# Kernel optimization log

Measured on AMD Instinct MI355X. Metric: run time of the kernel, lower is better.

## Reference

```python
import jax, jax.numpy as jnp
import numpy as np

B, N, CIN, C = 2, 400000, 192, 128
Y, X, Z = 512, 512, 40
EPS1 = 1e-5   # default BatchNorm1d eps for feature_proj
EPS2 = 1e-3   # norm_fn eps=0.001 for shared_conv BN


def setup_inputs() -> dict:
    key = jax.random.key(0)
    ks = jax.random.split(key, 12)
    voxel_features = jax.random.normal(ks[0], (N, CIN), jnp.float32)
    bi = jax.random.randint(ks[1], (N,), 0, B)
    zi = jax.random.randint(ks[2], (N,), 0, Z)
    yi = jax.random.randint(ks[3], (N,), 0, Y)
    xi = jax.random.randint(ks[4], (N,), 0, X)
    voxel_coords = jnp.stack([bi, zi, yi, xi], axis=1).astype(jnp.int32)  # (N,4)=[b,z,y,x]
    # feature_proj: Linear(CIN->C) + BN1d (inference stats) + ReLU
    W_proj = jax.random.normal(ks[5], (CIN, C), jnp.float32) * np.float32(1.0 / np.sqrt(CIN))
    b_proj = jnp.zeros((C,), jnp.float32)
    bn1_gamma = jnp.ones((C,), jnp.float32)
    bn1_beta = jnp.zeros((C,), jnp.float32)
    bn1_mean = jax.random.normal(ks[6], (C,), jnp.float32) * np.float32(0.1)
    bn1_var = jax.random.uniform(ks[7], (C,), jnp.float32, 0.5, 1.5)
    # shared_conv: SubMConv2d(C,C,3,pad=1,bias) + BN(eps=1e-3) + ReLU
    conv_w = jax.random.normal(ks[8], (3, 3, C, C), jnp.float32) * np.float32(1.0 / np.sqrt(9 * C))
    conv_b = jnp.zeros((C,), jnp.float32)
    bn2_gamma = jnp.ones((C,), jnp.float32)
    bn2_beta = jnp.zeros((C,), jnp.float32)
    bn2_mean = jax.random.normal(ks[9], (C,), jnp.float32) * np.float32(0.1)
    bn2_var = jax.random.uniform(ks[10], (C,), jnp.float32, 0.5, 1.5)
    return dict(voxel_features=voxel_features, voxel_coords=voxel_coords,
                W_proj=W_proj, b_proj=b_proj,
                bn1_gamma=bn1_gamma, bn1_beta=bn1_beta, bn1_mean=bn1_mean, bn1_var=bn1_var,
                conv_w=conv_w, conv_b=conv_b,
                bn2_gamma=bn2_gamma, bn2_beta=bn2_beta, bn2_mean=bn2_mean, bn2_var=bn2_var)


def reference(voxel_features, voxel_coords, W_proj, b_proj,
              bn1_gamma, bn1_beta, bn1_mean, bn1_var,
              conv_w, conv_b, bn2_gamma, bn2_beta, bn2_mean, bn2_var):
    # 1) feature_proj (Linear + BN1d inference + ReLU)
    f = voxel_features @ W_proj + b_proj                      # (N, C)
    f = (f - bn1_mean) * jax.lax.rsqrt(bn1_var + EPS1) * bn1_gamma + bn1_beta
    f = jax.nn.relu(f)
    # 2) bev_aggregate: unique([b,y,x]) + index_add == scatter-sum to dense BEV grid
    bi, yi, xi = voxel_coords[:, 0], voxel_coords[:, 2], voxel_coords[:, 3]
    dense = jnp.zeros((B, Y, X, C), f.dtype).at[bi, yi, xi].add(f)
    active = jnp.zeros((B, Y, X), bool).at[bi, yi, xi].set(True)
    # 3) SubMConv2d(3x3, pad=1) + BN + ReLU; subm == dense conv masked to active sites
    out = jax.lax.conv_general_dilated(dense, conv_w, (1, 1), 'SAME',
                                       dimension_numbers=('NHWC', 'HWIO', 'NHWC')) + conv_b
    out = (out - bn2_mean) * jax.lax.rsqrt(bn2_var + EPS2) * bn2_gamma + bn2_beta
    out = jax.nn.relu(out)
    # sparse tensor only holds active sites; zero elsewhere
    return jnp.where(active[..., None], out, jnp.float32(0.0))  # (B, Y, X, C)
```

## Files before the change

### kernel.cpp

```cpp
#include <hip/hip_runtime.h>

#define Bq 2
#define Yq 512
#define Xq 512
#define NVOX 400000

typedef __bf16 bf16x8 __attribute__((ext_vector_type(8)));
typedef float f32x4 __attribute__((ext_vector_type(4)));
typedef float f32x16 __attribute__((ext_vector_type(16)));
typedef short s16x8 __attribute__((ext_vector_type(8)));
typedef short s16x2 __attribute__((ext_vector_type(2)));

__device__ __forceinline__ short f2bf_s(float f){
    return __builtin_bit_cast(short, static_cast<__bf16>(f));
}

__device__ __forceinline__ void atomic_pk_add_bf16(short* addr, unsigned data){
#if __has_builtin(__builtin_amdgcn_global_atomic_fadd_v2bf16)
    s16x2 v; v[0] = (short)(data & 0xffff); v[1] = (short)(data >> 16);
    __builtin_amdgcn_global_atomic_fadd_v2bf16(
        (__attribute__((address_space(1))) s16x2*)addr, v);
#else
    asm volatile("global_atomic_pk_add_bf16 %0, %1, off"
                 :: "v"(addr), "v"(data) : "memory");
#endif
}

__global__ void kprep(const float* __restrict__ conv_w, const float* __restrict__ W_proj,
                      short* __restrict__ wTs, short* __restrict__ wpT){
    int tid = blockIdx.x*256 + threadIdx.x;
    if (tid < 9*128*128){
        int tap = tid >> 14; int r = tid & 16383; int co = r >> 7; int ci = r & 127;
        int g = ci >> 3, e = ci & 7;
        wTs[tap*16384 + co*128 + (((g & 8) | ((g & 7) ^ (co & 7))) << 3) + e] =
            f2bf_s(conv_w[tap*16384 + ci*128 + co]);
    }
    int e = tid - 9*128*128;
    if (e >= 0 && e < 128*192){
        int co = e / 192; int ci = e - co*192;
        wpT[e] = f2bf_s(W_proj[ci*128 + co]);
    }
}

__global__ void kcount(const int* __restrict__ vc, unsigned* __restrict__ cnt,
                       unsigned char* __restrict__ act){
    int i = blockIdx.x*256 + threadIdx.x;
    if (i >= NVOX) return;
    const int4 c = *reinterpret_cast<const int4*>(vc + i*4);
    int cell = (c.x*Yq + c.z)*Xq + c.w;
    act[cell] = 1;
    atomicAdd(&cnt[cell], 1u);
}

__global__ void __launch_bounds__(256, 4)
kproj(const float* __restrict__ vf, const int* __restrict__ vc,
      const unsigned* __restrict__ cnt,
      const short* __restrict__ wpT, const float* __restrict__ bp,
      const float* __restrict__ g1, const float* __restrict__ be1,
      const float* __restrict__ mu1, const float* __restrict__ va1,
      short* __restrict__ dbf){
    __shared__ char smem[64*200*2];
    __shared__ int cellsPk[64];
    short*    A  = (short*)smem;
    unsigned* st = (unsigned*)smem;
    const int t = threadIdx.x;
    const int v0 = blockIdx.x * 64;

    const float4* vf4 = reinterpret_cast<const float4*>(vf);
    #pragma unroll
    for (int j = 0; j < 12; ++j){
        int i = t + j*256;
        int v = i / 48, kq = i - v*48;
        float4 x = vf4[(size_t)(v0 + v)*48 + kq];
        short4 s; s.x=f2bf_s(x.x); s.y=f2bf_s(x.y); s.z=f2bf_s(x.z); s.w=f2bf_s(x.w);
        *reinterpret_cast<short4*>(&A[v*200 + kq*4]) = s;
    }
    if (t < 64){
        int vi = v0 + t;
        int bi = vc[vi*4 + 0], yi = vc[vi*4 + 2], xi = vc[vi*4 + 3];
        unsigned cn = cnt[(bi*Yq + yi)*Xq + xi];
        int P = (bi*514 + (yi + 1))*514 + (xi + 1);
        cellsPk[t] = (P*8 + ((xi + 1) & 7)) | ((cn > 1) ? (1 << 30) : 0);
    }
    __syncthreads();

    const int w  = t >> 6;
    const int l  = t & 63;
    const int lr = l & 15;
    const int q  = l >> 4;

    const short* wp_lane = wpT + (size_t)(w*32 + lr)*192 + q*8;
    bf16x8 bb[2][6];
    #pragma unroll
    for (int n = 0; n < 2; ++n)
        #pragma unroll
        for (int kc = 0; kc < 6; ++kc)
            bb[n][kc] = *reinterpret_cast<const bf16x8*>(wp_lane + n*16*192 + kc*32);

    f32x4 acc[4][2] = {};
    #pragma unroll
    for (int kc = 0; kc < 6; ++kc){
        bf16x8 a[4];
        #pragma unroll
        for (int m = 0; m < 4; ++m)
            a[m] = *reinterpret_cast<const bf16x8*>(&A[(m*16 + lr)*200 + kc*32 + q*8]);
        #pragma unroll
        for (int m = 0; m < 4; ++m)
            #pragma unroll
            for (int n = 0; n < 2; ++n)
                acc[m][n] = __builtin_amdgcn_mfma_f32_16x16x32_bf16(a[m], bb[n][kc], acc[m][n], 0, 0, 0);
    }

    __syncthreads();
    const int odd = lr & 1;
    #pragma unroll
    for (int n = 0; n < 2; ++n){
        int c = w*32 + n*16 + lr;
        float s1  = g1[c] * rsqrtf(va1[c] + 1e-5f);
        float sh1 = be1[c] + (bp[c] - mu1[c]) * s1;
        int jj = w*16 + n*8 + (lr >> 1);
        #pragma unroll
        for (int m = 0; m < 4; ++m){
            #pragma unroll
            for (int r = 0; r < 4; ++r){
                int vx = m*16 + q*4 + r;
                float val = fmaxf(fmaf(acc[m][n][r], s1, sh1), 0.f);
                float vp  = __shfl_xor(val, 1);
                if (!odd){
                    unsigned data = (unsigned)(unsigned short)f2bf_s(val)
                                  | ((unsigned)(unsigned short)f2bf_s(vp) << 16);
                    st[vx*68 + jj] = data;
                }
            }
        }
    }
    __syncthreads();

    unsigned* dbf_u32 = reinterpret_cast<unsigned*>(dbf);
    #pragma unroll
    for (int i = 0; i < 16; ++i){
        int vv = w*16 + i;
        int pk = cellsPk[vv];
        int multi = pk >> 30;
        int P = (pk & 0x3fffffff) >> 3, xp7 = pk & 7;
        unsigned data = st[vv*68 + l];
        size_t idx = (size_t)P*64 + (((l >> 2) ^ xp7) << 2) + (l & 3);
        if (multi){
            if (data) atomic_pk_add_bf16((short*)(dbf_u32 + idx), data);
        } else {
            dbf_u32[idx] = data;
        }
    }
}

__global__ void __launch_bounds__(512, 2)
kconv(const short* __restrict__ dbf, const short* __restrict__ wTs,
      const unsigned char* __restrict__ act, const float* __restrict__ cb,
      const float* __restrict__ g2, const float* __restrict__ be2,
      const float* __restrict__ mu2, const float* __restrict__ va2,
      float* __restrict__ out){
    __shared__ short Atile[5*1056*8];
    __shared__ short Bbuf[4][1024*8];
    const int t = threadIdx.x;
    const int bid = (blockIdx.x & 7)*256 + (blockIdx.x >> 3);
    const int b   = bid >> 10;
    const int rem = bid & 1023;
    const int y0  = (rem >> 3) << 2;
    const int x0  = (rem & 7) << 6;

    const int w   = t >> 6, l = t & 63;
    const int yy  = w >> 1, nn = w & 1;
    const int l31 = l & 31, hi = l >> 5;
    const int wbase16 = w*64*16;

    #define STAGE_B(BUF, H) do {                                              \
        const short* gb = wTs + (size_t)((H) >> 1)*16384 + ((H) & 1)*64;      \
        _Pragma("unroll")                                                     \
        for (int j = 0; j < 2; ++j){                                          \
            int S = j*512 + t;                                                \
            const short* gp = gb + (S >> 3)*128 + (S & 7)*8;                  \
            __builtin_amdgcn_global_load_lds(                                 \
                (const __attribute__((address_space(1))) void*)gp,            \
                (__attribute__((address_space(3))) void*)                    \
                    ((char*)Bbuf[BUF] + (size_t)(j*512*16) + wbase16), 16, 0, 0); \
        }                                                                     \
    } while(0)

    STAGE_B(0, 0);
    STAGE_B(1, 1);
    #pragma unroll
    for (int j = 0; j < 11; ++j){
        int S = j*512 + t;
        if (S < 5280){
            int r = S / 1056, s = S - r*1056;
            const short* gp = dbf + ((size_t)((b*514 + (y0 + r))*514 + x0)*16 + s)*8;
            __builtin_amdgcn_global_load_lds(
                (const __attribute__((address_space(1))) void*)gp,
                (__attribute__((address_space(3))) void*)
                    ((char*)Atile + (size_t)(j*512*16) + wbase16), 16, 0, 0);
        }
    }

    f32x16 acc[2][2] = {};
    const int bReadBase = (nn*64 + l31)*64;
    const int bXor = l31 & 7;

    #pragma unroll
    for (int p = 0; p < 18; ++p){
        if ((p & 1) == 0){
            __builtin_amdgcn_sched_barrier(0);
            asm volatile("s_waitcnt vmcnt(0)" ::: "memory");
            __builtin_amdgcn_s_barrier();
            __builtin_amdgcn_sched_barrier(0);
            if (p + 2 < 18) STAGE_B((p+2) & 3, p+2);
            if (p + 3 < 18) STAGE_B((p+3) & 3, p+3);
            if (p == 6){
                #pragma unroll
                for (int j = 0; j < 3; ++j){
                    int S = j*512 + t;
                    if (S < 1056){
                        const short* gp = dbf + ((size_t)((b*514 + (y0 + 5))*514 + x0)*16 + S)*8;
                        __builtin_amdgcn_global_load_lds(
                            (const __attribute__((address_space(1))) void*)gp,
                            (__attribute__((address_space(3))) void*)
                                ((char*)Atile + (size_t)(j*512 + w*64)*16), 16, 0, 0);
                    }
                }
            }
            __builtin_amdgcn_sched_barrier(0);
        }
        const short* Bc = Bbuf[p & 3];
        const int tap = p >> 1, hh = p & 1;
        const int ky = tap / 3, kx = tap - ky*3;
        const int row = yy + ky;
        const int rowp = (row >= 5) ? 0 : row;
        const int p0 = l31 + kx, p1 = p0 + 32;
        const int base0 = (rowp*1056 + p0*16)*8;
        const int base1 = (rowp*1056 + p1*16)*8;
        const int pk7 = p0 & 7;
        #pragma unroll
        for (int kc = 0; kc < 4; ++kc){
            const int ks  = kc*2 + hi;
            const int q   = ((hh*8 + ks) ^ pk7) << 3;
            const int qb  = (ks ^ bXor) << 3;
            bf16x8 a0 = *reinterpret_cast<const bf16x8*>(&Atile[base0 + q]);
            bf16x8 a1 = *reinterpret_cast<const bf16x8*>(&Atile[base1 + q]);
            bf16x8 b0 = *reinterpret_cast<const bf16x8*>(&Bc[bReadBase + qb]);
            bf16x8 b1 = *reinterpret_cast<const bf16x8*>(&Bc[bReadBase + 2048 + qb]);
            acc[0][0] = __builtin_amdgcn_mfma_f32_32x32x16_bf16(a0, b0, acc[0][0], 0, 0, 0);
            acc[0][1] = __builtin_amdgcn_mfma_f32_32x32x16_bf16(a0, b1, acc[0][1], 0, 0, 0);
            acc[1][0] = __builtin_amdgcn_mfma_f32_32x32x16_bf16(a1, b0, acc[1][0], 0, 0, 0);
            acc[1][1] = __builtin_amdgcn_mfma_f32_32x32x16_bf16(a1, b1, acc[1][1], 0, 0, 0);
        }
    }
    #undef STAGE_B

    const int yg = y0 + yy;
    const size_t rowcell = (size_t)(b*Yq + yg)*Xq + x0;
    #pragma unroll
    for (int ni = 0; ni < 2; ++ni){
        int c = nn*64 + ni*32 + l31;
        float s2  = g2[c] * rsqrtf(va2[c] + 1e-3f);
        float sh2 = be2[c] + (cb[c] - mu2[c]) * s2;
        #pragma unroll
        for (int mi = 0; mi < 2; ++mi){
            #pragma unroll
            for (int r = 0; r < 16; ++r){
                int pos = mi*32 + (r & 3) + ((r >> 2) << 3) + hi*4;
                size_t cell = rowcell + pos;
                float v = act[cell] ? fmaxf(fmaf(acc[mi][ni][r], s2, sh2), 0.f) : 0.f;
                out[cell*128 + c] = v;
            }
        }
    }
}

extern "C" void kernel_launch(void* const* d_in, const int* in_sizes, int n_in,
                              void* d_out, int out_size, void* d_ws, size_t ws_size,
                              hipStream_t stream){
    const float* vf  = (const float*)d_in[0];
    const int*   vc  = (const int*)  d_in[1];
    const float* Wp  = (const float*)d_in[2];
    const float* bp  = (const float*)d_in[3];
    const float* g1  = (const float*)d_in[4];
    const float* be1 = (const float*)d_in[5];
    const float* mu1 = (const float*)d_in[6];
    const float* va1 = (const float*)d_in[7];
    const float* cw  = (const float*)d_in[8];
    const float* cb  = (const float*)d_in[9];
    const float* g2  = (const float*)d_in[10];
    const float* be2 = (const float*)d_in[11];
    const float* mu2 = (const float*)d_in[12];
    const float* va2 = (const float*)d_in[13];
    float* out = (float*)d_out;
    char* ws = (char*)d_ws;

    if (ws_size < 138233856ull) return;
    short* dbf = (short*)ws;
    unsigned char* act = (unsigned char*)(ws + 135268352);
    short* wTs = (short*)(ws + 135792640);
    short* wpT = (short*)(ws + 136087552);
    unsigned* cnt = (unsigned*)(ws + 136136704);

    hipMemsetAsync(dbf, 0, 135268352, stream);
    hipMemsetAsync(act, 0, 524288, stream);
    hipMemsetAsync(cnt, 0, 2097152, stream);
    kprep<<<672, 256, 0, stream>>>(cw, Wp, wTs, wpT);
    kcount<<<1563, 256, 0, stream>>>(vc, cnt, act);
    kproj<<<6250, 256, 0, stream>>>(vf, vc, cnt, wpT, bp, g1, be1, mu1, va1, dbf);
    kconv<<<2048, 512, 0, stream>>>(dbf, wTs, act, cb, g2, be2, mu2, va2, out);
}
```

Measured before the change: 365.3 us.

## Replace bf16 atomic scatter with scratch slots and deterministic fixup reduction

Voxels that share a BEV cell no longer do packed-bf16 atomic adds into the dense grid. Each voxel gets a rank within its cell. The first voxel writes the grid directly and later duplicates write to per-cell scratch slots assigned by a new allocation kernel. A fixup kernel then sums the scratch rows into the grid in fp32 and rounds once. This removes atomic contention and repeated bf16 rounding, but adds two kernel launches, extra scratch traffic and a larger workspace requirement.

```diff
diff --git a/kernel.cpp b/kernel.cpp
--- a/kernel.cpp
+++ b/kernel.cpp
@@ -9,21 +9,12 @@
 typedef float f32x4 __attribute__((ext_vector_type(4)));
 typedef float f32x16 __attribute__((ext_vector_type(16)));
 typedef short s16x8 __attribute__((ext_vector_type(8)));
-typedef short s16x2 __attribute__((ext_vector_type(2)));
 
 __device__ __forceinline__ short f2bf_s(float f){
     return __builtin_bit_cast(short, static_cast<__bf16>(f));
 }
-
-__device__ __forceinline__ void atomic_pk_add_bf16(short* addr, unsigned data){
-#if __has_builtin(__builtin_amdgcn_global_atomic_fadd_v2bf16)
-    s16x2 v; v[0] = (short)(data & 0xffff); v[1] = (short)(data >> 16);
-    __builtin_amdgcn_global_atomic_fadd_v2bf16(
-        (__attribute__((address_space(1))) s16x2*)addr, v);
-#else
-    asm volatile("global_atomic_pk_add_bf16 %0, %1, off"
-                 :: "v"(addr), "v"(data) : "memory");
-#endif
+__device__ __forceinline__ float bfbits2f(unsigned u){
+    unsigned v = u << 16; return __builtin_bit_cast(float, v);
 }
 
 __global__ void kprep(const float* __restrict__ conv_w, const float* __restrict__ W_proj,
@@ -43,24 +34,38 @@
 }
 
 __global__ void kcount(const int* __restrict__ vc, unsigned* __restrict__ cnt,
-                       unsigned char* __restrict__ act){
+                       unsigned* __restrict__ vrank, unsigned char* __restrict__ act){
     int i = blockIdx.x*256 + threadIdx.x;
     if (i >= NVOX) return;
     const int4 c = *reinterpret_cast<const int4*>(vc + i*4);
     int cell = (c.x*Yq + c.z)*Xq + c.w;
     act[cell] = 1;
-    atomicAdd(&cnt[cell], 1u);
+    vrank[i] = atomicAdd(&cnt[cell], 1u);
+}
+
+__global__ void kalloc(const unsigned* __restrict__ cnt, unsigned* __restrict__ base,
+                       unsigned* __restrict__ mlist, unsigned* __restrict__ ctr){
+    int cell = blockIdx.x*256 + threadIdx.x;
+    if (cell >= Bq*Yq*Xq) return;
+    unsigned c = cnt[cell];
+    if (c > 1){
+        base[cell] = atomicAdd(&ctr[0], c - 1);
+        unsigned m  = atomicAdd(&ctr[1], 1);
+        mlist[m] = (unsigned)cell;
+    }
 }
 
 __global__ void __launch_bounds__(256, 4)
 kproj(const float* __restrict__ vf, const int* __restrict__ vc,
-      const unsigned* __restrict__ cnt,
+      const unsigned* __restrict__ cnt, const unsigned* __restrict__ vrank,
+      const unsigned* __restrict__ base,
       const short* __restrict__ wpT, const float* __restrict__ bp,
       const float* __restrict__ g1, const float* __restrict__ be1,
       const float* __restrict__ mu1, const float* __restrict__ va1,
-      short* __restrict__ dbf){
+      short* __restrict__ dbf, unsigned* __restrict__ scratch){
     __shared__ char smem[64*200*2];
     __shared__ int cellsPk[64];
+    __shared__ int slotArr[64];
     short*    A  = (short*)smem;
     unsigned* st = (unsigned*)smem;
     const int t = threadIdx.x;
@@ -78,9 +83,13 @@
     if (t < 64){
         int vi = v0 + t;
         int bi = vc[vi*4 + 0], yi = vc[vi*4 + 2], xi = vc[vi*4 + 3];
-        unsigned cn = cnt[(bi*Yq + yi)*Xq + xi];
+        int cell = (bi*Yq + yi)*Xq + xi;
+        unsigned cn = cnt[cell];
+        unsigned rk = vrank[vi];
         int P = (bi*514 + (yi + 1))*514 + (xi + 1);
-        cellsPk[t] = (P*8 + ((xi + 1) & 7)) | ((cn > 1) ? (1 << 30) : 0);
+        int toScratch = (cn > 1 && rk > 0) ? 1 : 0;
+        cellsPk[t] = (P*8 + ((xi + 1) & 7)) | (toScratch << 30);
+        slotArr[t] = toScratch ? (int)(base[cell] + rk - 1) : 0;
     }
     __syncthreads();
 
@@ -141,15 +150,43 @@
     for (int i = 0; i < 16; ++i){
         int vv = w*16 + i;
         int pk = cellsPk[vv];
-        int multi = pk >> 30;
-        int P = (pk & 0x3fffffff) >> 3, xp7 = pk & 7;
         unsigned data = st[vv*68 + l];
-        size_t idx = (size_t)P*64 + (((l >> 2) ^ xp7) << 2) + (l & 3);
-        if (multi){
-            if (data) atomic_pk_add_bf16((short*)(dbf_u32 + idx), data);
+        if (pk >> 30){
+            scratch[(size_t)slotArr[vv]*64 + l] = data;
         } else {
-            dbf_u32[idx] = data;
-        }
+            int P = (pk & 0x3fffffff) >> 3, xp7 = pk & 7;
+            dbf_u32[(size_t)P*64 + (((l >> 2) ^ xp7) << 2) + (l & 3)] = data;
+        }
+    }
+}
+
+__global__ void __launch_bounds__(256)
+kfix(const unsigned* __restrict__ mlist, const unsigned* __restrict__ ctr,
+     const unsigned* __restrict__ cnt, const unsigned* __restrict__ base,
+     const unsigned* __restrict__ scratch, unsigned* __restrict__ dbf_u32){
+    const unsigned nM = ctr[1];
+    const int l = threadIdx.x & 63;
+    const unsigned wid = (blockIdx.x*256 + threadIdx.x) >> 6;
+    const unsigned nw = gridDim.x * 4;
+    for (unsigned i = wid; i < nM; i += nw){
+        unsigned cell = mlist[i];
+        int x  = cell & 511;
+        int by = cell >> 9;
+        int b  = by >> 9, y = by & 511;
+        int P  = (b*514 + y + 1)*514 + (x + 1);
+        int xp7 = (x + 1) & 7;
+        unsigned c  = cnt[cell];
+        unsigned bs = base[cell];
+        size_t didx = (size_t)P*64 + (((l >> 2) ^ xp7) << 2) + (l & 3);
+        unsigned d = dbf_u32[didx];
+        float lo = bfbits2f(d & 0xffff), hi = bfbits2f(d >> 16);
+        for (unsigned r = 0; r + 1 < c; ++r){
+            unsigned s = scratch[(size_t)(bs + r)*64 + l];
+            lo += bfbits2f(s & 0xffff);
+            hi += bfbits2f(s >> 16);
+        }
+        dbf_u32[didx] = (unsigned)(unsigned short)f2bf_s(lo)
+                      | ((unsigned)(unsigned short)f2bf_s(hi) << 16);
     }
 }
 
@@ -295,18 +332,28 @@
     float* out = (float*)d_out;
     char* ws = (char*)d_ws;
 
-    if (ws_size < 138233856ull) return;
+    if (ws_size < 246428416ull) return;
     short* dbf = (short*)ws;
     unsigned char* act = (unsigned char*)(ws + 135268352);
     short* wTs = (short*)(ws + 135792640);
     short* wpT = (short*)(ws + 136087552);
-    unsigned* cnt = (unsigned*)(ws + 136136704);
+    unsigned* cnt   = (unsigned*)(ws + 136136704);
+    unsigned* vrank = (unsigned*)(ws + 138233856);
+    unsigned* base  = (unsigned*)(ws + 139833856);
+    unsigned* mlist = (unsigned*)(ws + 141931008);
+    unsigned* ctr   = (unsigned*)(ws + 144028160);
+    unsigned* scratch = (unsigned*)(ws + 144028416);
 
     hipMemsetAsync(dbf, 0, 135268352, stream);
     hipMemsetAsync(act, 0, 524288, stream);
     hipMemsetAsync(cnt, 0, 2097152, stream);
+    hipMemsetAsync(ctr, 0, 256, stream);
     kprep<<<672, 256, 0, stream>>>(cw, Wp, wTs, wpT);
-    kcount<<<1563, 256, 0, stream>>>(vc, cnt, act);
-    kproj<<<6250, 256, 0, stream>>>(vf, vc, cnt, wpT, bp, g1, be1, mu1, va1, dbf);
+    kcount<<<1563, 256, 0, stream>>>(vc, cnt, vrank, act);
+    kalloc<<<2048, 256, 0, stream>>>(cnt, base, mlist, ctr);
+    kproj<<<6250, 256, 0, stream>>>(vf, vc, cnt, vrank, base, wpT, bp,
+                                    g1, be1, mu1, va1, dbf, scratch);
+    kfix<<<2048, 256, 0, stream>>>(mlist, ctr, cnt, base, scratch,
+                                   (unsigned*)dbf);
     kconv<<<2048, 512, 0, stream>>>(dbf, wTs, act, cb, g2, be2, mu2, va2, out);
 }
```

New measurement: 580.0 us. +58.7%, slower.
